# Kernel optimization log

Hardware: AMD Instinct MI355X
Metric: run time of the kernel (lower is better)

Reference implementation:

```python
import jax, jax.numpy as jnp
import numpy as np

D_MODEL = 1024
EXPAND = 2
D_INNER = EXPAND * D_MODEL          # 2048
D_STATE = 64
NGROUPS = 1
HEADDIM = 128
NHEADS = D_INNER // HEADDIM         # 16
D_CONV = 4
CONV_DIM = D_INNER + 2 * NGROUPS * D_STATE      # 2176
D_IN_PROJ = 2 * D_INNER + 2 * NGROUPS * D_STATE + NHEADS  # 4240
BATCH = 2
SEQLEN = 4096
RMS_EPS = 1e-5


def setup_inputs() -> dict:
    key = jax.random.key(0)
    ks = jax.random.split(key, 8)
    u = jax.random.normal(ks[0], (BATCH, SEQLEN, D_MODEL), jnp.float32)
    in_proj_w = jax.random.normal(ks[1], (D_IN_PROJ, D_MODEL), jnp.float32) * 0.02
    conv_w = jax.random.normal(ks[2], (CONV_DIM, D_CONV), jnp.float32) * 0.2
    conv_b = jax.random.normal(ks[3], (CONV_DIM,), jnp.float32) * 0.1
    dt_bias = jax.random.normal(ks[4], (NHEADS,), jnp.float32) * 0.5
    # A ~ Uniform(1,16), A_log = log(A)  (as in Mamba2 init)
    A_log = jnp.log(jax.random.uniform(ks[5], (NHEADS,), jnp.float32, 1.0, 16.0))
    D = jnp.ones((NHEADS,), jnp.float32)
    rms_w = jnp.ones((D_INNER,), jnp.float32)
    out_w = jax.random.normal(ks[6], (D_MODEL, D_INNER), jnp.float32) * 0.02
    return {"u": u, "in_proj_w": in_proj_w, "conv_w": conv_w, "conv_b": conv_b,
            "dt_bias": dt_bias, "A_log": A_log, "D": D, "rms_w": rms_w, "out_w": out_w}


def reference(u, in_proj_w, conv_w, conv_b, dt_bias, A_log, D, rms_w, out_w):
    Bsz, L, _ = u.shape
    # in_proj: (B,L,d_model) -> (B,L,d_in_proj), split [z, x, B, C, dt]
    zxbcdt = jnp.einsum('bld,ed->ble', u, in_proj_w)
    s1 = D_INNER
    s2 = 2 * D_INNER
    s3 = s2 + NGROUPS * D_STATE
    s4 = s3 + NGROUPS * D_STATE
    z = zxbcdt[..., :s1]
    x = zxbcdt[..., s1:s2]
    B_part = zxbcdt[..., s2:s3]
    C_part = zxbcdt[..., s3:s4]
    dt = zxbcdt[..., s4:]
    dt = jax.nn.softplus(dt + dt_bias)            # (B,L,H), dt_limit=(0,inf) -> no clamp

    # depthwise causal conv1d + silu over [x, B, C]
    xBC = jnp.concatenate([x, B_part, C_part], axis=-1)      # (B,L,CONV_DIM)
    xt = xBC.transpose(0, 2, 1)                              # (B,C,L)
    kern = conv_w[:, None, :]                                # (C,1,W)
    conv = jax.lax.conv_general_dilated(
        xt, kern, (1,), [(D_CONV - 1, 0)],
        dimension_numbers=('NCH', 'OIH', 'NCH'),
        feature_group_count=CONV_DIM)
    xBC = jax.nn.silu((conv + conv_b[None, :, None]).transpose(0, 2, 1))

    x_c = xBC[..., :D_INNER]
    B_c = xBC[..., D_INNER:D_INNER + NGROUPS * D_STATE]
    C_c = xBC[..., D_INNER + NGROUPS * D_STATE:]
    x_s = x_c.reshape(Bsz, L, NHEADS, HEADDIM)               # (B,L,H,P)
    hpg = NHEADS // NGROUPS
    B_full = jnp.repeat(B_c.reshape(Bsz, L, NGROUPS, D_STATE), hpg, axis=2)  # (B,L,H,N)
    C_full = jnp.repeat(C_c.reshape(Bsz, L, NGROUPS, D_STATE), hpg, axis=2)

    A = -jnp.exp(A_log)                                      # (H,)

    def step(state, inp):
        x_t, dt_t, B_t, C_t = inp  # (B,H,P),(B,H),(B,H,N),(B,H,N)
        decay = jnp.exp(dt_t * A)[:, :, None, None]          # (B,H,1,1)
        state = decay * state + B_t[:, :, None, :] * x_t[..., None]  # (B,H,P,N)
        y_t = jnp.einsum('bhpn,bhn->bhp', state, C_t)
        return state, y_t

    init = jnp.zeros((Bsz, NHEADS, HEADDIM, D_STATE), u.dtype)
    xs = (x_s.transpose(1, 0, 2, 3), dt.transpose(1, 0, 2),
          B_full.transpose(1, 0, 2, 3), C_full.transpose(1, 0, 2, 3))
    _, ys = jax.lax.scan(step, init, xs)                     # (L,B,H,P)
    y = ys.transpose(1, 0, 2, 3) + D[None, None, :, None] * x_s

    y_flat = y.reshape(Bsz, L, D_INNER)
    mu = jnp.mean(y_flat * y_flat, axis=-1, keepdims=True)
    y_flat = y_flat * jax.lax.rsqrt(mu + RMS_EPS) * rms_w    # RMSNorm
    y_flat = y_flat * jax.nn.sigmoid(z)                      # gate
    return jnp.einsum('bld,ed->ble', y_flat, out_w)          # out_proj (no bias)
```

## Files before the change

### kernel.cpp

```cpp
#include <hip/hip_runtime.h>
#include <math.h>

#define D_MODEL   1024
#define D_INNER   2048
#define D_STATE   64
#define HEADDIM   128
#define NHEADS    16
#define D_CONV    4
#define BATCH     2
#define SEQLEN    4096
#define RMS_EPS   1e-5f
#define D_IN_PROJ 4240

#define ZX_LD     4224

#define LCHUNK    128
#define NCHUNK    (SEQLEN / LCHUNK)

typedef __attribute__((ext_vector_type(8))) short short8;
typedef __attribute__((ext_vector_type(4))) float f32x4;
typedef _Float16 half8 __attribute__((ext_vector_type(8)));

__device__ __forceinline__ ushort f2bf(float f) {
  unsigned u = __float_as_uint(f);
  u += 0x7fff + ((u >> 16) & 1);
  return (ushort)(u >> 16);
}
__device__ __forceinline__ float bf2f(ushort h) {
  return __uint_as_float(((unsigned)h) << 16);
}
__device__ __forceinline__ ushort f2h(float f) {
  _Float16 h = (_Float16)f;
  ushort u; __builtin_memcpy(&u, &h, 2); return u;
}
__device__ __forceinline__ void ld4(const float* p, float* d) {
  float4 v = *(const float4*)p; d[0] = v.x; d[1] = v.y; d[2] = v.z; d[3] = v.w;
}
__device__ __forceinline__ void ld4b(const ushort* p, float* d) {
  ushort4 v = *(const ushort4*)p;
  d[0] = bf2f(v.x); d[1] = bf2f(v.y); d[2] = bf2f(v.z); d[3] = bf2f(v.w);
}

__device__ __forceinline__ void gl_lds16(const ushort* g, ushort* l) {
  __builtin_amdgcn_global_load_lds(
      (const __attribute__((address_space(1))) unsigned int*)g,
      (__attribute__((address_space(3))) unsigned int*)l, 16, 0, 0);
}

__global__ void cvt_split(const float* __restrict__ w,
                          ushort* __restrict__ hi, ushort* __restrict__ lo, int n4) {
  int i = blockIdx.x * 256 + threadIdx.x;
  if (i >= n4) return;
  float4 v = ((const float4*)w)[i];
  ushort h0 = f2bf(v.x), h1 = f2bf(v.y), h2 = f2bf(v.z), h3 = f2bf(v.w);
  ushort l0 = f2bf(v.x - bf2f(h0)), l1 = f2bf(v.y - bf2f(h1));
  ushort l2 = f2bf(v.z - bf2f(h2)), l3 = f2bf(v.w - bf2f(h3));
  ((ushort4*)hi)[i] = make_ushort4(h0, h1, h2, h3);
  ((ushort4*)lo)[i] = make_ushort4(l0, l1, l2, l3);
}

__global__ void cvt_f16(const float* __restrict__ w, ushort* __restrict__ o, int n4) {
  int i = blockIdx.x * 256 + threadIdx.x;
  if (i >= n4) return;
  float4 v = ((const float4*)w)[i];
  ((ushort4*)o)[i] = make_ushort4(f2h(v.x), f2h(v.y), f2h(v.z), f2h(v.w));
}

__global__ void cvt_u3(const float* __restrict__ w, ushort* __restrict__ hi,
                       ushort* __restrict__ lo, ushort* __restrict__ h16, int n4) {
  int i = blockIdx.x * 256 + threadIdx.x;
  if (i >= n4) return;
  float4 v = ((const float4*)w)[i];
  ushort h0 = f2bf(v.x), h1 = f2bf(v.y), h2 = f2bf(v.z), h3 = f2bf(v.w);
  ((ushort4*)hi)[i]  = make_ushort4(h0, h1, h2, h3);
  ((ushort4*)lo)[i]  = make_ushort4(f2bf(v.x - bf2f(h0)), f2bf(v.y - bf2f(h1)),
                                    f2bf(v.z - bf2f(h2)), f2bf(v.w - bf2f(h3)));
  ((ushort4*)h16)[i] = make_ushort4(f2h(v.x), f2h(v.y), f2h(v.z), f2h(v.w));
}

template<int BM, int BK, bool ALO, bool OBF16>
__launch_bounds__(256, 3)
__global__ void gemm_bf16p(const ushort* __restrict__ Ah, const ushort* __restrict__ Al,
                           const ushort* __restrict__ Bh, const ushort* __restrict__ Bl,
                           float* __restrict__ C, int ldc,
                           int M, int N, int ldab, int Kslice, int n1term) {
  constexpr int BN = 128;
  constexpr int NQ = BK / 8;
  constexpr int RT = BM / 32;
  constexpr int CT = 4;
  constexpr int KS = BK / 32;

  __shared__ ushort As[ALO ? 2 : 1][BM * BK];
  __shared__ ushort Bs[2][BN * BK];

  const int bn   = blockIdx.x * BN;
  if (bn >= N) return;
  const bool two = (bn >= n1term);
  const int t    = threadIdx.x;
  const int bm   = blockIdx.y * BM;
  const int kz   = blockIdx.z;
  const int kb   = kz * Kslice;
  C += (size_t)kz * M * ldc;
  const int wave = t >> 6, lane = t & 63;
  const int ml   = lane & 15, g4 = lane >> 4;
  const int sw   = ml & (NQ - 1);
  const int wr   = wave & 1, wc = wave >> 1;
  const int r0   = wr * RT * 16, c0 = wc * CT * 16;

  f32x4 acc[RT][CT];
#pragma unroll
  for (int i = 0; i < RT; ++i)
#pragma unroll
    for (int j = 0; j < CT; ++j) acc[i][j] = (f32x4){0.f, 0.f, 0.f, 0.f};

  for (int k0 = kb; k0 < kb + Kslice; k0 += BK) {
    __syncthreads();
#pragma unroll
    for (int ii = 0; ii < BM * NQ / 256; ++ii) {
      int idx = t + ii * 256;
      int row = idx / NQ, qs = idx % NQ;
      int qg  = qs ^ (row & (NQ - 1));
      size_t go = (size_t)(bm + row) * ldab + k0 + qg * 8;
      gl_lds16(Ah + go, &As[0][idx * 8]);
      if (ALO) gl_lds16(Al + go, &As[ALO ? 1 : 0][idx * 8]);
    }
#pragma unroll
    for (int ii = 0; ii < BN * NQ / 256; ++ii) {
      int idx = t + ii * 256;
      int row = idx / NQ, qs = idx % NQ;
      int qg  = qs ^ (row & (NQ - 1));
      size_t go = (size_t)(bn + row) * ldab + k0 + qg * 8;
      gl_lds16(Bh + go, &Bs[0][idx * 8]);
      if (two) gl_lds16(Bl + go, &Bs[1][idx * 8]);
    }
    __syncthreads();

#pragma unroll
    for (int ks = 0; ks < KS; ++ks) {
      const int qA = ((ks * 4 + g4) ^ sw) * 8;
      short8 ah[RT], al[RT], bh[CT], bl[CT];
#pragma unroll
      for (int i = 0; i < RT; ++i) {
        int off = (r0 + i * 16 + ml) * BK + qA;
        ah[i] = *(const short8*)&As[0][off];
        if (ALO) al[i] = *(const short8*)&As[ALO ? 1 : 0][off];
      }
#pragma unroll
      for (int j = 0; j < CT; ++j) {
        int off = (c0 + j * 16 + ml) * BK + qA;
        bh[j] = *(const short8*)&Bs[0][off];
        if (two) bl[j] = *(const short8*)&Bs[1][off];
      }
#pragma unroll
      for (int i = 0; i < RT; ++i)
#pragma unroll
        for (int j = 0; j < CT; ++j) {
          acc[i][j] = __builtin_amdgcn_mfma_f32_16x16x32_bf16(ah[i], bh[j], acc[i][j], 0, 0, 0);
          if (two)
            acc[i][j] = __builtin_amdgcn_mfma_f32_16x16x32_bf16(ah[i], bl[j], acc[i][j], 0, 0, 0);
          if (ALO)
            acc[i][j] = __builtin_amdgcn_mfma_f32_16x16x32_bf16(al[i], bh[j], acc[i][j], 0, 0, 0);
        }
    }
  }

#pragma unroll
  for (int i = 0; i < RT; ++i)
#pragma unroll
    for (int j = 0; j < CT; ++j) {
      int col = bn + c0 + j * 16 + ml;
      if (col < N) {
        int rowb = bm + r0 + i * 16 + g4 * 4;
#pragma unroll
        for (int r = 0; r < 4; ++r) {
          if (OBF16) ((ushort*)C)[(size_t)(rowb + r) * ldc + col] = f2bf(acc[i][j][r]);
          else       C[(size_t)(rowb + r) * ldc + col] = acc[i][j][r];
        }
      }
    }
}

template<int BM, int BK, bool OBF16, bool PIPE>
__launch_bounds__(256, PIPE ? 2 : 4)
__global__ void gemm_f16(const ushort* __restrict__ Ah, const ushort* __restrict__ Bh,
                         float* __restrict__ C, int ldc,
                         int M, int N, int ldab, int Kslice) {
  constexpr int BN = 128;
  constexpr int NQ = BK / 8;
  constexpr int RT = BM / 32;
  constexpr int CT = 4;
  constexpr int KS = BK / 32;
  constexpr int NBUF = PIPE ? 2 : 1;

  __shared__ ushort As[NBUF][BM * BK];
  __shared__ ushort Bs[NBUF][BN * BK];

  const int bn   = blockIdx.x * BN;
  if (bn >= N) return;
  const int t    = threadIdx.x;
  const int bm   = blockIdx.y * BM;
  const int kz   = blockIdx.z;
  const int kb   = kz * Kslice;
  C += (size_t)kz * M * ldc;
  const int wave = t >> 6, lane = t & 63;
  const int ml   = lane & 15, g4 = lane >> 4;
  const int sw   = ml & (NQ - 1);
  const int wr   = wave & 1, wc = wave >> 1;
  const int r0   = wr * RT * 16, c0 = wc * CT * 16;

  f32x4 acc[RT][CT];
#pragma unroll
  for (int i = 0; i < RT; ++i)
#pragma unroll
    for (int j = 0; j < CT; ++j) acc[i][j] = (f32x4){0.f, 0.f, 0.f, 0.f};

  auto stage = [&](int k0, int buf) {
#pragma unroll
    for (int ii = 0; ii < BM * NQ / 256; ++ii) {
      int idx = t + ii * 256;
      int row = idx / NQ, qs = idx % NQ;
      int qg  = qs ^ (row & (NQ - 1));
      size_t go = (size_t)(bm + row) * ldab + k0 + qg * 8;
      gl_lds16(Ah + go, &As[buf][idx * 8]);
    }
#pragma unroll
    for (int ii = 0; ii < BN * NQ / 256; ++ii) {
      int idx = t + ii * 256;
      int row = idx / NQ, qs = idx % NQ;
      int qg  = qs ^ (row & (NQ - 1));
      size_t go = (size_t)(bn + row) * ldab + k0 + qg * 8;
      gl_lds16(Bh + go, &Bs[buf][idx * 8]);
    }
  };

  auto compute = [&](int buf) {
#pragma unroll
    for (int ks = 0; ks < KS; ++ks) {
      const int qA = ((ks * 4 + g4) ^ sw) * 8;
      half8 ah[RT], bh[CT];
#pragma unroll
      for (int i = 0; i < RT; ++i)
        ah[i] = *(const half8*)&As[buf][(r0 + i * 16 + ml) * BK + qA];
#pragma unroll
      for (int j = 0; j < CT; ++j)
        bh[j] = *(const half8*)&Bs[buf][(c0 + j * 16 + ml) * BK + qA];
#pragma unroll
      for (int i = 0; i < RT; ++i)
#pragma unroll
        for (int j = 0; j < CT; ++j)
          acc[i][j] = __builtin_amdgcn_mfma_f32_16x16x32_f16(ah[i], bh[j], acc[i][j], 0, 0, 0);
    }
  };

  if (PIPE) {
    const int NIT = Kslice / BK;
    stage(kb, 0);
    if (NIT > 1) stage(kb + BK, 1);
    for (int it = 0; it < NIT; ++it) {
      const int buf = it & 1;
      if (it + 1 < NIT) asm volatile("s_waitcnt vmcnt(8)" ::: "memory");
      else              asm volatile("s_waitcnt vmcnt(0)" ::: "memory");
      __builtin_amdgcn_s_barrier();
      __builtin_amdgcn_sched_barrier(0);
      compute(buf);
      __builtin_amdgcn_sched_barrier(0);
      __builtin_amdgcn_s_barrier();
      __builtin_amdgcn_sched_barrier(0);
      if (it + 2 < NIT) stage(kb + (it + 2) * BK, buf);
    }
  } else {
    for (int k0 = kb; k0 < kb + Kslice; k0 += BK) {
      __syncthreads();
      stage(k0, 0);
      __syncthreads();
      compute(0);
    }
  }

#pragma unroll
  for (int i = 0; i < RT; ++i)
#pragma unroll
    for (int j = 0; j < CT; ++j) {
      int col = bn + c0 + j * 16 + ml;
      if (col < N) {
        int rowb = bm + r0 + i * 16 + g4 * 4;
#pragma unroll
        for (int r = 0; r < 4; ++r) {
          if (OBF16) ((ushort*)C)[(size_t)(rowb + r) * ldc + col] = f2bf(acc[i][j][r]);
          else       C[(size_t)(rowb + r) * ldc + col] = acc[i][j][r];
        }
      }
    }
}

__global__ void add_out(const float* __restrict__ P, float* __restrict__ out, int n4) {
  int i = blockIdx.x * 256 + threadIdx.x;
  if (i >= n4) return;
  float4 a = ((const float4*)P)[i];
  float4 b = ((const float4*)(P + (size_t)SEQLEN * D_MODEL))[i];
  ((float4*)out)[i] = make_float4(a.x + b.x, a.y + b.y, a.z + b.z, a.w + b.w);
}

__global__ void add_dt(const float* __restrict__ P, float* __restrict__ dtb) {
  int i = blockIdx.x * 256 + threadIdx.x;
  if (i >= SEQLEN * NHEADS / 4) return;
  float4 s = ((const float4*)P)[i];
#pragma unroll
  for (int k = 1; k < 8; ++k) {
    float4 v = ((const float4*)(P + (size_t)k * SEQLEN * NHEADS))[i];
    s.x += v.x; s.y += v.y; s.z += v.z; s.w += v.w;
  }
  ((float4*)dtb)[i] = s;
}


__device__ __forceinline__ void cum_scan(float* cum, float v, int t, float* carry) {
  int lane = t & 63;
#pragma unroll
  for (int off = 1; off < 64; off <<= 1) {
    float o = __shfl_up(v, off);
    if (lane >= off) v += o;
  }
  if (t == 63) *carry = v;
  __syncthreads();
  if (t >= 64 && t < LCHUNK) v += *carry;
  if (t < LCHUNK) cum[t] = v;
  __syncthreads();
}

__device__ __forceinline__ void conv4b(const ushort* __restrict__ zx,
                                       const float* __restrict__ cw,
                                       const float* __restrict__ cb,
                                       int l, int col0, float* outv) {
  const ushort* bp = zx + (size_t)l * ZX_LD + col0;
  float r3[4], r2[4], r1[4], r0[4], bb[4];
  ld4b(bp, r3);
  if (l >= 1) ld4b(bp - ZX_LD, r2);     else { r2[0]=r2[1]=r2[2]=r2[3]=0.f; }
  if (l >= 2) ld4b(bp - 2 * ZX_LD, r1); else { r1[0]=r1[1]=r1[2]=r1[3]=0.f; }
  if (l >= 3) ld4b(bp - 3 * ZX_LD, r0); else { r0[0]=r0[1]=r0[2]=r0[3]=0.f; }
  const int ch = col0 - 2048;
  ld4(cb + ch, bb);
#pragma unroll
  for (int j = 0; j < 4; ++j) {
    float w4[4]; ld4(cw + (ch + j) * 4, w4);
    float a = bb[j];
    a = fmaf(w4[0], r0[j], a);
    a = fmaf(w4[1], r1[j], a);
    a = fmaf(w4[2], r2[j], a);
    a = fmaf(w4[3], r3[j], a);
    outv[j] = a / (1.f + __expf(-a));
  }
}

__launch_bounds__(256, 2)
__global__ void passA_ssd(const ushort* __restrict__ zx,
                          const float* __restrict__ dtb,
                          const float* __restrict__ cw, const float* __restrict__ cb,
                          const float* __restrict__ dt_bias,
                          const float* __restrict__ A_log,
                          float* __restrict__ Sc, float* __restrict__ Pc,
                          float* __restrict__ xconv, float* __restrict__ bconv) {
  const int blk = blockIdx.x;
  const int c   = blk & (NCHUNK - 1);
  const int h   = blk >> 5;
  const int l0  = c * LCHUNK;
  const int t   = threadIdx.x;
  const int wave = t >> 6, lane = t & 63;
  const int ml = lane & 15, g4 = lane >> 4;
  const float Ah = -expf(A_log[h]);

  __shared__ float cum[LCHUNK];
  __shared__ float carry;
  __shared__ ushort Xt[LCHUNK * 40];
  __shared__ ushort Bt[D_STATE * 40];

  {
    float v = 0.f;
    if (t < LCHUNK) {
      float xv = dtb[(size_t)(l0 + t) * NHEADS + h] + dt_bias[h];
      float sp = (xv > 20.f) ? xv : log1pf(expf(xv));
      v = sp * Ah;
    }
    cum_scan(cum, v, t, &carry);
  }
  const float cend = cum[LCHUNK - 1];

  f32x4 acc[2][4];
#pragma unroll
  for (int i = 0; i < 2; ++i)
#pragma unroll
    for (int j = 0; j < 4; ++j) acc[i][j] = (f32x4){0.f, 0.f, 0.f, 0.f};
  const int p0 = wave * 32;

  for (int slab = 0; slab < 4; ++slab) {
    __syncthreads();
    for (int i = 0; i < 4; ++i) {
      int q = t + i * 256;
      int s = q >> 5, p4 = (q & 31) * 4;
      int l = l0 + slab * 32 + s;
      float xv[4];
      conv4b(zx, cw, cb, l, 2048 + h * HEADDIM + p4, xv);
      *(float4*)(xconv + (size_t)l * D_INNER + h * HEADDIM + p4) =
          make_float4(xv[0], xv[1], xv[2], xv[3]);
#pragma unroll
      for (int j = 0; j < 4; ++j) Xt[(p4 + j) * 40 + s] = f2h(xv[j]);
    }
    for (int i = 0; i < 2; ++i) {
      int q = t + i * 256;
      int s = q >> 4, n4 = (q & 15) * 4;
      int l = l0 + slab * 32 + s;
      float wd = __expf(cend - cum[slab * 32 + s]);
      float bv[4];
      conv4b(zx, cw, cb, l, 4096 + n4, bv);
      if (h == 0)
        *(float4*)(bconv + (size_t)l * D_STATE + n4) =
            make_float4(bv[0], bv[1], bv[2], bv[3]);
#pragma unroll
      for (int j = 0; j < 4; ++j) Bt[(n4 + j) * 40 + s] = f2h(bv[j] * wd);
    }
    __syncthreads();

    half8 xa[2];
#pragma unroll
    for (int pi = 0; pi < 2; ++pi)
      xa[pi] = *(const half8*)&Xt[(p0 + pi * 16 + ml) * 40 + g4 * 8];
#pragma unroll
    for (int ni = 0; ni < 4; ++ni) {
      half8 bh = *(const half8*)&Bt[(ni * 16 + ml) * 40 + g4 * 8];
#pragma unroll
      for (int pi = 0; pi < 2; ++pi)
        acc[pi][ni] = __builtin_amdgcn_mfma_f32_16x16x32_f16(xa[pi], bh, acc[pi][ni], 0, 0, 0);
    }
  }

  float* S = Sc + (size_t)blk * (HEADDIM * D_STATE);
#pragma unroll
  for (int pi = 0; pi < 2; ++pi)
#pragma unroll
    for (int ni = 0; ni < 4; ++ni) {
      int n = ni * 16 + ml;
#pragma unroll
      for (int r = 0; r < 4; ++r) {
        int p = p0 + pi * 16 + g4 * 4 + r;
        S[(size_t)p * D_STATE + n] = acc[pi][ni][r];
      }
    }
  if (t == 0) Pc[blk] = __expf(cend);
}

__global__ void scan_passB(float* __restrict__ Sc, const float* __restrict__ Pc) {
  const int h = blockIdx.x;
  const int e = blockIdx.y * 512 + threadIdx.x;
  const size_t hb = (size_t)h * NCHUNK;
  float st = 0.f;
  for (int c = 0; c < NCHUNK; ++c) {
    size_t idx = (hb + c) * (HEADDIM * D_STATE) + e;
    float P = Pc[hb + c];
    float v = Sc[idx];
    Sc[idx] = st;
    st = fmaf(P, st, v);
  }
}

__launch_bounds__(256, 2)
__global__ void passC_ssd(const ushort* __restrict__ zx,
                          const float* __restrict__ dtb,
                          const float* __restrict__ cw, const float* __restrict__ cb,
                          const float* __restrict__ dt_bias,
                          const float* __restrict__ A_log,
                          const float* __restrict__ Dp,
                          const float* __restrict__ Sc,
                          const float* __restrict__ bconv,
                          float* __restrict__ ybuf) {
  const int blk = blockIdx.x;
  const int c   = blk & (NCHUNK - 1);
  const int h   = blk >> 5;
  const int l0  = c * LCHUNK;
  const int t   = threadIdx.x;
  const int wave = t >> 6, lane = t & 63;
  const int ml = lane & 15, g4 = lane >> 4;
  const int t0 = wave * 32;
  const float Ah = -expf(A_log[h]);
  const float Dh = Dp[h];

  __shared__ float cum[LCHUNK];
  __shared__ float carry;
  __shared__ ushort ldsb[12800];
  ushort* Bsl0 = ldsb;
  ushort* Bsl1 = ldsb + 1280;
  ushort* Msl  = ldsb + 2560;
  ushort* Xt   = ldsb + 7680;

  {
    float v = 0.f;
    if (t < LCHUNK) {
      float xv = dtb[(size_t)(l0 + t) * NHEADS + h] + dt_bias[h];
      float sp = (xv > 20.f) ? xv : log1pf(expf(xv));
      v = sp * Ah;
    }
    cum_scan(cum, v, t, &carry);
  }

  half8 cf[2][2];
  {
    ushort* CS = ldsb;
    int row = t >> 1, half_ = t & 1;
    int l = l0 + row;
    int colbase = 4160 + half_ * 32;
#pragma unroll
    for (int j0 = 0; j0 < 32; j0 += 4) {
      float cv[4];
      conv4b(zx, cw, cb, l, colbase + j0, cv);
      int colc = half_ * 32 + j0;
      int quad = colc >> 3;
      int addr = row * 64 + ((quad ^ (row & 7)) << 3) + (colc & 7);
      *(ushort4*)&CS[addr] = make_ushort4(f2h(cv[0]), f2h(cv[1]), f2h(cv[2]), f2h(cv[3]));
    }
    __syncthreads();
#pragma unroll
    for (int ks = 0; ks < 2; ++ks)
#pragma unroll
      for (int ti = 0; ti < 2; ++ti) {
        int rw = t0 + ti * 16 + ml;
        int ad = rw * 64 + (((ks * 4 + g4) ^ (rw & 7)) << 3);
        cf[ks][ti] = *(const half8*)&CS[ad];
      }
  }

  f32x4 accY[2][8];
#pragma unroll
  for (int i = 0; i < 2; ++i)
#pragma unroll
    for (int j = 0; j < 8; ++j) accY[i][j] = (f32x4){0.f, 0.f, 0.f, 0.f};

  const float* xcv = ybuf;

  for (int slab = 0; slab < 4; ++slab) {
    __syncthreads();
#pragma unroll
    for (int i = 0; i < 2; ++i) {
      int q = t + i * 256;
      int s = q >> 4, n4 = (q & 15) * 4;
      int l = l0 + slab * 32 + s;
      float4 v = *(const float4*)(bconv + (size_t)l * D_STATE + n4);
      ushort* B = (n4 < 32) ? Bsl0 : Bsl1;
      int jj = n4 & 31;
      *(ushort4*)&B[s * 40 + jj] = make_ushort4(f2h(v.x), f2h(v.y), f2h(v.z), f2h(v.w));
    }
#pragma unroll
    for (int i = 0; i < 4; ++i) {
      int q = t + i * 256;
      int p = q & 127, sg = q >> 7;
      ushort hh[4];
#pragma unroll
      for (int j = 0; j < 4; ++j) {
        int l = l0 + slab * 32 + sg * 4 + j;
        hh[j] = f2h(xcv[(size_t)l * D_INNER + h * HEADDIM + p]);
      }
      *(ushort4*)&Xt[p * 40 + sg * 4] = make_ushort4(hh[0], hh[1], hh[2], hh[3]);
    }
    __syncthreads();

    if (wave >= slab) {
      f32x4 g[2][2];
#pragma unroll
      for (int i = 0; i < 2; ++i)
#pragma unroll
        for (int j = 0; j < 2; ++j) g[i][j] = (f32x4){0.f, 0.f, 0.f, 0.f};
#pragma unroll
      for (int ks = 0; ks < 2; ++ks) {
        const ushort* B = ks ? Bsl1 : Bsl0;
#pragma unroll
        for (int si = 0; si < 2; ++si) {
          half8 bh = *(const half8*)&B[(si * 16 + ml) * 40 + g4 * 8];
#pragma unroll
          for (int ti = 0; ti < 2; ++ti)
            g[ti][si] = __builtin_amdgcn_mfma_f32_16x16x32_f16(cf[ks][ti], bh, g[ti][si], 0, 0, 0);
        }
      }
#pragma unroll
      for (int ti = 0; ti < 2; ++ti)
#pragma unroll
        for (int si = 0; si < 2; ++si) {
          int sl = si * 16 + ml;
          int sg = slab * 32 + sl;
#pragma unroll
          for (int r = 0; r < 4; ++r) {
            int tg = t0 + ti * 16 + g4 * 4 + r;
            float coeff = (sg <= tg) ? __expf(cum[tg] - cum[sg]) : 0.f;
            float val = g[ti][si][r] * coeff + ((sg == tg) ? Dh : 0.f);
            Msl[tg * 40 + sl] = f2h(val);
          }
        }
      asm volatile("s_waitcnt lgkmcnt(0)" ::: "memory");
      half8 ma[2];
#pragma unroll
      for (int ti = 0; ti < 2; ++ti)
        ma[ti] = *(const half8*)&Msl[(t0 + ti * 16 + ml) * 40 + g4 * 8];
#pragma unroll
      for (int pi = 0; pi < 8; ++pi) {
        half8 xh = *(const half8*)&Xt[(pi * 16 + ml) * 40 + g4 * 8];
#pragma unroll
        for (int ti = 0; ti < 2; ++ti)
          accY[ti][pi] = __builtin_amdgcn_mfma_f32_16x16x32_f16(ma[ti], xh, accY[ti][pi], 0, 0, 0);
      }
    }
  }

  const float* S = Sc + (size_t)blk * (HEADDIM * D_STATE);
#pragma unroll
  for (int ns = 0; ns < 2; ++ns) {
    __syncthreads();
#pragma unroll
    for (int i = 0; i < 4; ++i) {
      int q = t + i * 256;
      int p = q >> 3, j4 = (q & 7) * 4;
      float4 v = *(const float4*)(S + (size_t)p * D_STATE + ns * 32 + j4);
      *(ushort4*)&Xt[p * 40 + j4] = make_ushort4(f2h(v.x), f2h(v.y), f2h(v.z), f2h(v.w));
    }
    __syncthreads();
    half8 ma[2];
#pragma unroll
    for (int ti = 0; ti < 2; ++ti) {
      float e = __expf(cum[t0 + ti * 16 + ml]);
#pragma unroll
      for (int j = 0; j < 8; ++j)
        ma[ti][j] = (_Float16)((float)cf[ns][ti][j] * e);
    }
#pragma unroll
    for (int pi = 0; pi < 8; ++pi) {
      half8 xh = *(const half8*)&Xt[(pi * 16 + ml) * 40 + g4 * 8];
#pragma unroll
      for (int ti = 0; ti < 2; ++ti)
        accY[ti][pi] = __builtin_amdgcn_mfma_f32_16x16x32_f16(ma[ti], xh, accY[ti][pi], 0, 0, 0);
    }
  }

#pragma unroll
  for (int ti = 0; ti < 2; ++ti)
#pragma unroll
    for (int pi = 0; pi < 8; ++pi) {
      int p = pi * 16 + ml;
#pragma unroll
      for (int r = 0; r < 4; ++r) {
        int l = l0 + t0 + ti * 16 + g4 * 4 + r;
        ybuf[(size_t)l * D_INNER + h * HEADDIM + p] = accY[ti][pi][r];
      }
    }
}

__launch_bounds__(256)
__global__ void rmsnorm_gate_split(const float* __restrict__ ybuf,
                                   const ushort* __restrict__ zx,
                                   const float* __restrict__ rms_w,
                                   ushort* __restrict__ yh) {
  const int row = blockIdx.x;
  const int t   = threadIdx.x;
  const float* y  = ybuf + (size_t)row * D_INNER;
  const ushort* z = zx   + (size_t)row * ZX_LD;

  float4 a  = *(const float4*)(y + t * 8);
  float4 bq = *(const float4*)(y + t * 8 + 4);
  float ss = a.x * a.x + a.y * a.y + a.z * a.z + a.w * a.w +
             bq.x * bq.x + bq.y * bq.y + bq.z * bq.z + bq.w * bq.w;
#pragma unroll
  for (int off = 32; off > 0; off >>= 1) ss += __shfl_down(ss, off);
  __shared__ float red[4];
  if ((t & 63) == 0) red[t >> 6] = ss;
  __syncthreads();
  float tot = red[0] + red[1] + red[2] + red[3];
  float scale = rsqrtf(tot * (1.f / (float)D_INNER) + RMS_EPS);

  float vy[8] = {a.x, a.y, a.z, a.w, bq.x, bq.y, bq.z, bq.w};
  ushort4 zv0 = *(const ushort4*)(z + t * 8);
  ushort4 zv1 = *(const ushort4*)(z + t * 8 + 4);
  ushort zz[8] = {zv0.x, zv0.y, zv0.z, zv0.w, zv1.x, zv1.y, zv1.z, zv1.w};
  ushort hh[8];
#pragma unroll
  for (int jj = 0; jj < 8; ++jj) {
    int col = t * 8 + jj;
    float g = 1.f / (1.f + __expf(-bf2f(zz[jj])));
    float v = vy[jj] * scale * rms_w[col] * g;
    hh[jj] = f2h(v);
  }
  size_t o = (size_t)row * D_INNER + t * 8;
  *(ushort4*)(yh + o)     = make_ushort4(hh[0], hh[1], hh[2], hh[3]);
  *(ushort4*)(yh + o + 4) = make_ushort4(hh[4], hh[5], hh[6], hh[7]);
}

extern "C" void kernel_launch(void* const* d_in, const int* in_sizes, int n_in,
                              void* d_out, int out_size, void* d_ws, size_t ws_size,
                              hipStream_t stream) {
  const float* u         = (const float*)d_in[0];
  const float* in_proj_w = (const float*)d_in[1];
  const float* conv_w    = (const float*)d_in[2];
  const float* conv_b    = (const float*)d_in[3];
  const float* dt_bias   = (const float*)d_in[4];
  const float* A_log     = (const float*)d_in[5];
  const float* Dp        = (const float*)d_in[6];
  const float* rms_w     = (const float*)d_in[7];
  const float* out_w     = (const float*)d_in[8];
  float* out = (float*)d_out;

  float* ws    = (float*)d_ws;
  ushort* zxbc = (ushort*)ws;
  float* dtb   = ws   + (size_t)SEQLEN * ZX_LD / 2;
  float* dtp   = dtb  + (size_t)SEQLEN * NHEADS;
  float* ybuf  = dtp  + (size_t)8 * SEQLEN * NHEADS;
  float* Pc    = ybuf + (size_t)SEQLEN * D_INNER;
  float* Sc    = Pc   + 512;
  ushort* uh   = (ushort*)(Sc + (size_t)NHEADS * NCHUNK * HEADDIM * D_STATE);
  ushort* ul   = uh  + (size_t)SEQLEN * D_MODEL;
  ushort* w1h  = ul  + (size_t)SEQLEN * D_MODEL;
  ushort* w1l  = w1h + (size_t)D_IN_PROJ * D_MODEL;
  ushort* w2h  = w1l + (size_t)D_IN_PROJ * D_MODEL;
  ushort* w2l  = w2h + (size_t)D_MODEL * D_INNER;
  ushort* yh   = (ushort*)Sc;
  float* Opart = ybuf;
  float* bconv = dtp;
  ushort* uf16 = (ushort*)ybuf;

  {
    int n4 = D_IN_PROJ * D_MODEL / 4;
    cvt_split<<<(n4 + 255) / 256, 256, 0, stream>>>(in_proj_w, w1h, w1l, n4);
    int z4 = ZX_LD * D_MODEL / 4;
    cvt_f16<<<(z4 + 255) / 256, 256, 0, stream>>>(in_proj_w, w1h, z4);
    int m4 = D_MODEL * D_INNER / 4;
    cvt_f16<<<(m4 + 255) / 256, 256, 0, stream>>>(out_w, w2h, m4);
  }

  for (int b = 0; b < BATCH; ++b) {
    const float* u_b  = u   + (size_t)b * SEQLEN * D_MODEL;
    float*      out_b = out + (size_t)b * SEQLEN * D_MODEL;

    {
      int n4 = SEQLEN * D_MODEL / 4;
      cvt_u3<<<(n4 + 255) / 256, 256, 0, stream>>>(u_b, uh, ul, uf16, n4);
    }

    {
      dim3 g(40, SEQLEN / 128, 1);
      gemm_f16<128, 64, true, false><<<g, 256, 0, stream>>>(uf16, w1h, (float*)zxbc,
                                                            ZX_LD, SEQLEN, ZX_LD,
                                                            D_MODEL, D_MODEL);
    }
    {
      const ushort* bh = w1h + (size_t)ZX_LD * D_MODEL;
      const ushort* bl = w1l + (size_t)ZX_LD * D_MODEL;
      dim3 g(1, SEQLEN / 128, 8);
      gemm_bf16p<128, 32, true, false><<<g, 256, 0, stream>>>(uh, ul, bh, bl,
                                                          dtp, NHEADS, SEQLEN, NHEADS,
                                                          D_MODEL, D_MODEL / 8, 0);
      add_dt<<<(SEQLEN * NHEADS / 4 + 255) / 256, 256, 0, stream>>>(dtp, dtb);
    }

    passA_ssd<<<NHEADS * NCHUNK, 256, 0, stream>>>(zxbc, dtb, conv_w, conv_b,
                                                   dt_bias, A_log, Sc, Pc,
                                                   ybuf, bconv);
    scan_passB<<<dim3(NHEADS, (HEADDIM * D_STATE) / 512), 512, 0, stream>>>(Sc, Pc);
    passC_ssd<<<NHEADS * NCHUNK, 256, 0, stream>>>(zxbc, dtb, conv_w, conv_b,
                                                   dt_bias, A_log, Dp, Sc,
                                                   bconv, ybuf);

    rmsnorm_gate_split<<<SEQLEN, 256, 0, stream>>>(ybuf, zxbc, rms_w, yh);

    {
      dim3 g(D_MODEL / 128, SEQLEN / 128, 2);
      gemm_f16<128, 64, false, true><<<g, 256, 0, stream>>>(yh, w2h, Opart, D_MODEL,
                                                            SEQLEN, D_MODEL,
                                                            D_INNER, D_INNER / 2);
    }
    add_out<<<(SEQLEN * D_MODEL / 4 + 255) / 256, 256, 0, stream>>>(Opart, out_b,
                                                                    SEQLEN * D_MODEL / 4);
  }
}
```

Measured before the change: 464.3 us.

## Split SSD chunk kernels across two headdim halves to double grid size

passA_ssd and passC_ssd now launch a second grid dimension that splits the 128-wide head dimension into two 64-wide halves. This doubles the block count from 512 to 1024 and shrinks per-block LDS and accumulator registers, and launch bounds are raised to 4 blocks per CU. The aim is better occupancy and CU fill. The cost is redundant work per half: the dt cumulative scan, the B conv and the C conv plus the CB mask computation are all repeated.

After: 462.1 us. No clear change (-0.5%).

```diff
diff --git a/kernel.cpp b/kernel.cpp
--- a/kernel.cpp
+++ b/kernel.cpp
@@ -352,7 +352,7 @@
   }
 }
 
-__launch_bounds__(256, 2)
+__launch_bounds__(256, 4)
 __global__ void passA_ssd(const ushort* __restrict__ zx,
                           const float* __restrict__ dtb,
                           const float* __restrict__ cw, const float* __restrict__ cb,
@@ -363,6 +363,8 @@
   const int blk = blockIdx.x;
   const int c   = blk & (NCHUNK - 1);
   const int h   = blk >> 5;
+  const int ph  = blockIdx.y;
+  const int pbase = ph * 64;
   const int l0  = c * LCHUNK;
   const int t   = threadIdx.x;
   const int wave = t >> 6, lane = t & 63;
@@ -371,7 +373,7 @@
 
   __shared__ float cum[LCHUNK];
   __shared__ float carry;
-  __shared__ ushort Xt[LCHUNK * 40];
+  __shared__ ushort Xt[64 * 40];
   __shared__ ushort Bt[D_STATE * 40];
 
   {
@@ -385,22 +387,20 @@
   }
   const float cend = cum[LCHUNK - 1];
 
-  f32x4 acc[2][4];
-#pragma unroll
-  for (int i = 0; i < 2; ++i)
-#pragma unroll
-    for (int j = 0; j < 4; ++j) acc[i][j] = (f32x4){0.f, 0.f, 0.f, 0.f};
-  const int p0 = wave * 32;
+  f32x4 acc[4];
+#pragma unroll
+  for (int j = 0; j < 4; ++j) acc[j] = (f32x4){0.f, 0.f, 0.f, 0.f};
+  const int p0 = wave * 16;
 
   for (int slab = 0; slab < 4; ++slab) {
     __syncthreads();
-    for (int i = 0; i < 4; ++i) {
+    for (int i = 0; i < 2; ++i) {
       int q = t + i * 256;
-      int s = q >> 5, p4 = (q & 31) * 4;
+      int s = q >> 4, p4 = (q & 15) * 4;
       int l = l0 + slab * 32 + s;
       float xv[4];
-      conv4b(zx, cw, cb, l, 2048 + h * HEADDIM + p4, xv);
-      *(float4*)(xconv + (size_t)l * D_INNER + h * HEADDIM + p4) =
+      conv4b(zx, cw, cb, l, 2048 + h * HEADDIM + pbase + p4, xv);
+      *(float4*)(xconv + (size_t)l * D_INNER + h * HEADDIM + pbase + p4) =
           make_float4(xv[0], xv[1], xv[2], xv[3]);
 #pragma unroll
       for (int j = 0; j < 4; ++j) Xt[(p4 + j) * 40 + s] = f2h(xv[j]);
@@ -412,7 +412,7 @@
       float wd = __expf(cend - cum[slab * 32 + s]);
       float bv[4];
       conv4b(zx, cw, cb, l, 4096 + n4, bv);
-      if (h == 0)
+      if (h == 0 && ph == 0)
         *(float4*)(bconv + (size_t)l * D_STATE + n4) =
             make_float4(bv[0], bv[1], bv[2], bv[3]);
 #pragma unroll
@@ -420,32 +420,25 @@
     }
     __syncthreads();
 
-    half8 xa[2];
-#pragma unroll
-    for (int pi = 0; pi < 2; ++pi)
-      xa[pi] = *(const half8*)&Xt[(p0 + pi * 16 + ml) * 40 + g4 * 8];
+    half8 xa = *(const half8*)&Xt[(p0 + ml) * 40 + g4 * 8];
 #pragma unroll
     for (int ni = 0; ni < 4; ++ni) {
       half8 bh = *(const half8*)&Bt[(ni * 16 + ml) * 40 + g4 * 8];
-#pragma unroll
-      for (int pi = 0; pi < 2; ++pi)
-        acc[pi][ni] = __builtin_amdgcn_mfma_f32_16x16x32_f16(xa[pi], bh, acc[pi][ni], 0, 0, 0);
+      acc[ni] = __builtin_amdgcn_mfma_f32_16x16x32_f16(xa, bh, acc[ni], 0, 0, 0);
     }
   }
 
   float* S = Sc + (size_t)blk * (HEADDIM * D_STATE);
 #pragma unroll
-  for (int pi = 0; pi < 2; ++pi)
-#pragma unroll
-    for (int ni = 0; ni < 4; ++ni) {
-      int n = ni * 16 + ml;
-#pragma unroll
-      for (int r = 0; r < 4; ++r) {
-        int p = p0 + pi * 16 + g4 * 4 + r;
-        S[(size_t)p * D_STATE + n] = acc[pi][ni][r];
-      }
-    }
-  if (t == 0) Pc[blk] = __expf(cend);
+  for (int ni = 0; ni < 4; ++ni) {
+    int n = ni * 16 + ml;
+#pragma unroll
+    for (int r = 0; r < 4; ++r) {
+      int p = pbase + p0 + g4 * 4 + r;
+      S[(size_t)p * D_STATE + n] = acc[ni][r];
+    }
+  }
+  if (t == 0 && ph == 0) Pc[blk] = __expf(cend);
 }
 
 __global__ void scan_passB(float* __restrict__ Sc, const float* __restrict__ Pc) {
@@ -462,7 +455,7 @@
   }
 }
 
-__launch_bounds__(256, 2)
+__launch_bounds__(256, 4)
 __global__ void passC_ssd(const ushort* __restrict__ zx,
                           const float* __restrict__ dtb,
                           const float* __restrict__ cw, const float* __restrict__ cb,
@@ -475,6 +468,8 @@
   const int blk = blockIdx.x;
   const int c   = blk & (NCHUNK - 1);
   const int h   = blk >> 5;
+  const int ph  = blockIdx.y;
+  const int pbase = ph * 64;
   const int l0  = c * LCHUNK;
   const int t   = threadIdx.x;
   const int wave = t >> 6, lane = t & 63;
@@ -485,7 +480,7 @@
 
   __shared__ float cum[LCHUNK];
   __shared__ float carry;
-  __shared__ ushort ldsb[12800];
+  __shared__ ushort ldsb[10240];
   ushort* Bsl0 = ldsb;
   ushort* Bsl1 = ldsb + 1280;
   ushort* Msl  = ldsb + 2560;
@@ -527,11 +522,11 @@
       }
   }
 
-  f32x4 accY[2][8];
+  f32x4 accY[2][4];
 #pragma unroll
   for (int i = 0; i < 2; ++i)
 #pragma unroll
-    for (int j = 0; j < 8; ++j) accY[i][j] = (f32x4){0.f, 0.f, 0.f, 0.f};
+    for (int j = 0; j < 4; ++j) accY[i][j] = (f32x4){0.f, 0.f, 0.f, 0.f};
 
   const float* xcv = ybuf;
 
@@ -548,14 +543,14 @@
       *(ushort4*)&B[s * 40 + jj] = make_ushort4(f2h(v.x), f2h(v.y), f2h(v.z), f2h(v.w));
     }
 #pragma unroll
-    for (int i = 0; i < 4; ++i) {
+    for (int i = 0; i < 2; ++i) {
       int q = t + i * 256;
-      int p = q & 127, sg = q >> 7;
+      int p = q & 63, sg = q >> 6;
       ushort hh[4];
 #pragma unroll
       for (int j = 0; j < 4; ++j) {
         int l = l0 + slab * 32 + sg * 4 + j;
-        hh[j] = f2h(xcv[(size_t)l * D_INNER + h * HEADDIM + p]);
+        hh[j] = f2h(xcv[(size_t)l * D_INNER + h * HEADDIM + pbase + p]);
       }
       *(ushort4*)&Xt[p * 40 + sg * 4] = make_ushort4(hh[0], hh[1], hh[2], hh[3]);
     }
@@ -598,7 +593,7 @@
       for (int ti = 0; ti < 2; ++ti)
         ma[ti] = *(const half8*)&Msl[(t0 + ti * 16 + ml) * 40 + g4 * 8];
 #pragma unroll
-      for (int pi = 0; pi < 8; ++pi) {
+      for (int pi = 0; pi < 4; ++pi) {
         half8 xh = *(const half8*)&Xt[(pi * 16 + ml) * 40 + g4 * 8];
 #pragma unroll
         for (int ti = 0; ti < 2; ++ti)
@@ -612,10 +607,10 @@
   for (int ns = 0; ns < 2; ++ns) {
     __syncthreads();
 #pragma unroll
-    for (int i = 0; i < 4; ++i) {
+    for (int i = 0; i < 2; ++i) {
       int q = t + i * 256;
       int p = q >> 3, j4 = (q & 7) * 4;
-      float4 v = *(const float4*)(S + (size_t)p * D_STATE + ns * 32 + j4);
+      float4 v = *(const float4*)(S + (size_t)(pbase + p) * D_STATE + ns * 32 + j4);
       *(ushort4*)&Xt[p * 40 + j4] = make_ushort4(f2h(v.x), f2h(v.y), f2h(v.z), f2h(v.w));
     }
     __syncthreads();
@@ -628,7 +623,7 @@
         ma[ti][j] = (_Float16)((float)cf[ns][ti][j] * e);
     }
 #pragma unroll
-    for (int pi = 0; pi < 8; ++pi) {
+    for (int pi = 0; pi < 4; ++pi) {
       half8 xh = *(const half8*)&Xt[(pi * 16 + ml) * 40 + g4 * 8];
 #pragma unroll
       for (int ti = 0; ti < 2; ++ti)
@@ -639,8 +634,8 @@
 #pragma unroll
   for (int ti = 0; ti < 2; ++ti)
 #pragma unroll
-    for (int pi = 0; pi < 8; ++pi) {
-      int p = pi * 16 + ml;
+    for (int pi = 0; pi < 4; ++pi) {
+      int p = pbase + pi * 16 + ml;
 #pragma unroll
       for (int r = 0; r < 4; ++r) {
         int l = l0 + t0 + ti * 16 + g4 * 4 + r;
@@ -754,13 +749,13 @@
       add_dt<<<(SEQLEN * NHEADS / 4 + 255) / 256, 256, 0, stream>>>(dtp, dtb);
     }
 
-    passA_ssd<<<NHEADS * NCHUNK, 256, 0, stream>>>(zxbc, dtb, conv_w, conv_b,
-                                                   dt_bias, A_log, Sc, Pc,
-                                                   ybuf, bconv);
+    passA_ssd<<<dim3(NHEADS * NCHUNK, 2), 256, 0, stream>>>(zxbc, dtb, conv_w, conv_b,
+                                                            dt_bias, A_log, Sc, Pc,
+                                                            ybuf, bconv);
     scan_passB<<<dim3(NHEADS, (HEADDIM * D_STATE) / 512), 512, 0, stream>>>(Sc, Pc);
-    passC_ssd<<<NHEADS * NCHUNK, 256, 0, stream>>>(zxbc, dtb, conv_w, conv_b,
-                                                   dt_bias, A_log, Dp, Sc,
-                                                   bconv, ybuf);
+    passC_ssd<<<dim3(NHEADS * NCHUNK, 2), 256, 0, stream>>>(zxbc, dtb, conv_w, conv_b,
+                                                            dt_bias, A_log, Dp, Sc,
+                                                            bconv, ybuf);
 
     rmsnorm_gate_split<<<SEQLEN, 256, 0, stream>>>(ybuf, zxbc, rms_w, yh);
 
```
